# Performance work log

Measured on AMD Instinct MI355X. Metric: run time of the kernel, lower is better.

## Reference

```python
import jax, jax.numpy as jnp
import numpy as np

NUM_HEADS = 8
H_NUM, W_NUM = 1, 2   # idx=0 stripe windows
SCALE = float((256 // NUM_HEADS) ** -0.5)  # qk_scale


def _partition(x, h_sp, w_sp):
    # x: (T,B,C,H,W) -> (T, B*nWin, heads, N, C//heads) with N = h_sp*w_sp
    T, B, C, H, W = x.shape
    x = x.reshape(T, B, C, H // h_sp, h_sp, W // w_sp, w_sp)
    x = x.transpose(0, 1, 3, 5, 4, 6, 2)  # T,B,nH,nW,h_sp,w_sp,C
    x = x.reshape(T, -1, h_sp * w_sp, NUM_HEADS, C // NUM_HEADS)
    return x.transpose(0, 1, 3, 2, 4)


def setup_inputs() -> dict:
    key = jax.random.key(0)
    k1, k2, k3 = jax.random.split(key, 3)
    shape = (4, 2, 256, 56, 56)
    return {
        "q": jax.random.normal(k1, shape, jnp.float32),
        "k": jax.random.normal(k2, shape, jnp.float32),
        "v": jax.random.normal(k3, shape, jnp.float32),
        "v_lamda": 1,
    }


def reference(q, k, v, v_lamda):
    T, B, C, H0, W0 = q.shape
    h_pad = (-H0) % H_NUM
    w_pad = (-W0) % W_NUM
    pad = ((0, 0), (0, 0), (0, 0), (0, h_pad), (0, w_pad))
    q = jnp.pad(q, pad)
    k = jnp.pad(k, pad)
    v = jnp.pad(v, pad)
    H, W = H0 + h_pad, W0 + w_pad
    h_sp, w_sp = H // H_NUM, W // W_NUM

    qw = _partition(q, h_sp, w_sp)  # (T, BnW, h, N, d)
    kw = _partition(k, h_sp, w_sp)
    vw = _partition(v, h_sp, w_sp)  # head dim = C*v_lamda//heads

    attn = jnp.einsum('twhnd,twhmd->twhnm', qw, kw)          # (QK^T), no softmax
    out = jnp.einsum('twhnm,twhmd->twhnd', attn, vw) * (SCALE * 2)

    # merge windows back: (T,BnW,h,N,d) -> (T,B,Cv,H,W)
    Cv = C * v_lamda
    out = out.transpose(0, 1, 3, 2, 4).reshape(T, -1, h_sp * w_sp, Cv)
    out = out.reshape(T, B, H_NUM, W_NUM, h_sp, w_sp, Cv)
    out = out.transpose(0, 1, 2, 4, 3, 5, 6).reshape(T, B, H, W, Cv)
    out = out.transpose(0, 1, 4, 2, 3)
    return out[:, :, :, :H0, :W0]
```

## Files before the change

### kernel.cpp

```cpp
#include <hip/hip_runtime.h>


#define HW 3136
#define WDIM 56
#define SPLIT 14
#define PSPLIT 112
#define SCALE2 0.35355339059327373f

typedef const __attribute__((address_space(1))) void gas_void;
typedef __attribute__((address_space(3))) void las_void;
typedef float v2f __attribute__((ext_vector_type(2)));

__global__ __launch_bounds__(256, 4) void kv_kernel(const float* __restrict__ K,
                                                    const float* __restrict__ V,
                                                    float* __restrict__ Mpart) {
    __shared__ float lds[2 * 32 * PSPLIT];

    const int blk = blockIdx.x;
    const int p   = blk / SPLIT;
    const int s   = blk - p * SPLIT;
    const int head = p & 7;
    const int win  = (p >> 3) & 1;
    const int b    = (p >> 4) & 1;
    const int t    = p >> 5;

    const size_t base = (size_t)((t * 2 + b) * 256 + head * 32) * HW;
    const float* __restrict__ Kb = K + base;
    const float* __restrict__ Vb = V + base;

    const int tid = threadIdx.x;
    const int l   = tid & 63;
    const int w   = tid >> 6;

    #pragma unroll
    for (int i = 0; i < 7; ++i) {
        const int q    = (w * 7 + i) * 64 + l;
        const int isv  = q >= 896 ? 1 : 0;
        const int r    = q - isv * 896;
        const int pq   = r >> 5;
        const int slot = r & 31;
        const int ch   = ((slot & 7) << 2) + (slot >> 3);
        const int n    = s * PSPLIT + pq * 4;
        const int y    = n / 28;
        const int x    = n - y * 28;
        const float* src = (isv ? Vb : Kb)
                         + (size_t)ch * HW + y * WDIM + win * 28 + x;
        float* dst = &lds[(w * 7 + i) * 256];
        __builtin_amdgcn_global_load_lds((gas_void*)src, (las_void*)dst, 16, 0, 0);
    }
    __syncthreads();

    const int gg = l >> 3;
    const int e  = l & 7;

    v2f acc2[4][4] = {};
    #pragma unroll
    for (int j = 0; j < 7; ++j) {
        const int rowb = (7 * w + j) * 128;
        float4 ka[4], va[4];
        #pragma unroll
        for (int i = 0; i < 4; ++i) {
            ka[i] = *(const float4*)&lds[rowb + (gg + 8 * i) * 4];
            va[i] = *(const float4*)&lds[3584 + rowb + (e + 8 * i) * 4];
        }
        #pragma unroll
        for (int i = 0; i < 4; ++i) {
            const v2f ka_lo = {ka[i].x, ka[i].y};
            const v2f ka_hi = {ka[i].z, ka[i].w};
            #pragma unroll
            for (int jj = 0; jj < 4; ++jj) {
                const v2f va_lo = {va[jj].x, va[jj].y};
                const v2f va_hi = {va[jj].z, va[jj].w};
                acc2[i][jj] += ka_lo * va_lo;
                acc2[i][jj] += ka_hi * va_hi;
            }
        }
    }
    __syncthreads();

    const int dd0 = gg * 4;
    const int de0 = e * 4;
    #pragma unroll
    for (int i = 0; i < 4; ++i)
        #pragma unroll
        for (int jj = 0; jj < 4; ++jj)
            lds[w * 1024 + (dd0 + i) * 32 + (de0 + jj)] = acc2[i][jj].x + acc2[i][jj].y;
    __syncthreads();

    const float4 r0 = *(const float4*)&lds[tid * 4];
    const float4 r1 = *(const float4*)&lds[1024 + tid * 4];
    const float4 r2 = *(const float4*)&lds[2048 + tid * 4];
    const float4 r3 = *(const float4*)&lds[3072 + tid * 4];
    float4 o;
    o.x = r0.x + r1.x + r2.x + r3.x;
    o.y = r0.y + r1.y + r2.y + r3.y;
    o.z = r0.z + r1.z + r2.z + r3.z;
    o.w = r0.w + r1.w + r2.w + r3.w;
    *(float4*)&Mpart[(size_t)blk * 1024 + tid * 4] = o;
}

__global__ __launch_bounds__(256, 4) void qm_kernel(const float* __restrict__ Q,
                                                    const float* __restrict__ Mpart,
                                                    float* __restrict__ Out) {
    __shared__ float M[1024];
    const int blk = blockIdx.x;
    const int p   = blk / 7;
    const int c   = blk - p * 7;
    const int tid = threadIdx.x;

    const int head = p & 7;
    const int win  = (p >> 3) & 1;
    const int b    = (p >> 4) & 1;
    const int t    = p >> 5;

    const float* __restrict__ Qb = nullptr;
    float*       __restrict__ Ob = nullptr;
    float qv[32];
    if (tid < 224) {
        const int n = c * 224 + tid;
        const int y = n / 28;
        const int x = n - y * 28;
        const size_t base = (size_t)((t * 2 + b) * 256 + head * 32) * HW
                          + y * WDIM + win * 28 + x;
        Qb = Q + base;
        Ob = Out + base;
        #pragma unroll
        for (int dd = 0; dd < 32; ++dd)
            qv[dd] = Qb[(size_t)dd * HW];
    }

    const float* mp = Mpart + (size_t)p * SPLIT * 1024 + tid * 4;
    v2f s0 = {0.f, 0.f}, s1 = {0.f, 0.f};
    #pragma unroll
    for (int s = 0; s < SPLIT; ++s) {
        const float4 v = *(const float4*)&mp[s * 1024];
        const v2f vlo = {v.x, v.y};
        const v2f vhi = {v.z, v.w};
        s0 += vlo; s1 += vhi;
    }
    float4 sum;
    sum.x = s0.x * SCALE2; sum.y = s0.y * SCALE2;
    sum.z = s1.x * SCALE2; sum.w = s1.y * SCALE2;
    *(float4*)&M[tid * 4] = sum;
    __syncthreads();

    if (tid < 224) {
        v2f acc2[16] = {};
        #pragma unroll 8
        for (int dd = 0; dd < 32; ++dd) {
            const v2f qq = {qv[dd], qv[dd]};
            #pragma unroll
            for (int g4 = 0; g4 < 8; ++g4) {
                const float4 m = *(const float4*)&M[dd * 32 + g4 * 4];
                const v2f mlo = {m.x, m.y};
                const v2f mhi = {m.z, m.w};
                acc2[g4 * 2 + 0] += qq * mlo;
                acc2[g4 * 2 + 1] += qq * mhi;
            }
        }
        #pragma unroll
        for (int g4 = 0; g4 < 8; ++g4) {
            Ob[(size_t)(g4 * 4 + 0) * HW] = acc2[g4 * 2 + 0].x;
            Ob[(size_t)(g4 * 4 + 1) * HW] = acc2[g4 * 2 + 0].y;
            Ob[(size_t)(g4 * 4 + 2) * HW] = acc2[g4 * 2 + 1].x;
            Ob[(size_t)(g4 * 4 + 3) * HW] = acc2[g4 * 2 + 1].y;
        }
    }
}

extern "C" void kernel_launch(void* const* d_in, const int* in_sizes, int n_in,
                              void* d_out, int out_size, void* d_ws, size_t ws_size,
                              hipStream_t stream) {
    const float* q = (const float*)d_in[0];
    const float* k = (const float*)d_in[1];
    const float* v = (const float*)d_in[2];
    float* out   = (float*)d_out;
    float* Mpart = (float*)d_ws;

    kv_kernel<<<128 * SPLIT, 256, 0, stream>>>(k, v, Mpart);
    qm_kernel<<<128 * 7, 256, 0, stream>>>(q, Mpart, out);
}
```

Measured before the change: 127.8 us.

## Double KV split count, and process two pixels per thread in Q·M kernel

The K·V reduction kernel now splits each window-head into 28 chunks of 56 pixels instead of 14 chunks of 112, doubling its block count and halving its LDS footprint. The load and compute loops are reshaped to match. The second kernel now has each thread handle two adjacent pixels with 8-byte vector loads and stores, and uses 4 blocks per window-head instead of 7. The aim is more parallelism in the first kernel and wider memory accesses in the second, at the cost of twice as many partial sums to reduce and more registers per thread.

```diff
diff --git a/kernel.cpp b/kernel.cpp
--- a/kernel.cpp
+++ b/kernel.cpp
@@ -3,18 +3,18 @@
 
 #define HW 3136
 #define WDIM 56
-#define SPLIT 14
-#define PSPLIT 112
+#define SPLIT 28
+#define PSPLIT 56
 #define SCALE2 0.35355339059327373f
 
 typedef const __attribute__((address_space(1))) void gas_void;
 typedef __attribute__((address_space(3))) void las_void;
 typedef float v2f __attribute__((ext_vector_type(2)));
 
-__global__ __launch_bounds__(256, 4) void kv_kernel(const float* __restrict__ K,
-                                                    const float* __restrict__ V,
-                                                    float* __restrict__ Mpart) {
-    __shared__ float lds[2 * 32 * PSPLIT];
+__global__ __launch_bounds__(256) void kv_kernel(const float* __restrict__ K,
+                                                 const float* __restrict__ V,
+                                                 float* __restrict__ Mpart) {
+    __shared__ float lds[4096];
 
     const int blk = blockIdx.x;
     const int p   = blk / SPLIT;
@@ -33,20 +33,22 @@
     const int w   = tid >> 6;
 
     #pragma unroll
-    for (int i = 0; i < 7; ++i) {
-        const int q    = (w * 7 + i) * 64 + l;
-        const int isv  = q >= 896 ? 1 : 0;
-        const int r    = q - isv * 896;
-        const int pq   = r >> 5;
-        const int slot = r & 31;
-        const int ch   = ((slot & 7) << 2) + (slot >> 3);
-        const int n    = s * PSPLIT + pq * 4;
-        const int y    = n / 28;
-        const int x    = n - y * 28;
-        const float* src = (isv ? Vb : Kb)
-                         + (size_t)ch * HW + y * WDIM + win * 28 + x;
-        float* dst = &lds[(w * 7 + i) * 256];
-        __builtin_amdgcn_global_load_lds((gas_void*)src, (las_void*)dst, 16, 0, 0);
+    for (int i = 0; i < 4; ++i) {
+        if (i < 3 || w < 2) {
+            const int q    = i * 256 + tid;
+            const int isv  = q >= 448 ? 1 : 0;
+            const int r    = q - isv * 448;
+            const int pq   = r >> 5;
+            const int slot = r & 31;
+            const int ch   = ((slot & 7) << 2) + (slot >> 3);
+            const int n    = s * PSPLIT + pq * 4;
+            const int y    = n / 28;
+            const int x    = n - y * 28;
+            const float* src = (isv ? Vb : Kb)
+                             + (size_t)ch * HW + y * WDIM + win * 28 + x;
+            float* dst = &lds[i * 1024 + w * 256];
+            __builtin_amdgcn_global_load_lds((gas_void*)src, (las_void*)dst, 16, 0, 0);
+        }
     }
     __syncthreads();
 
@@ -55,24 +57,27 @@
 
     v2f acc2[4][4] = {};
     #pragma unroll
-    for (int j = 0; j < 7; ++j) {
-        const int rowb = (7 * w + j) * 128;
-        float4 ka[4], va[4];
-        #pragma unroll
-        for (int i = 0; i < 4; ++i) {
-            ka[i] = *(const float4*)&lds[rowb + (gg + 8 * i) * 4];
-            va[i] = *(const float4*)&lds[3584 + rowb + (e + 8 * i) * 4];
-        }
-        #pragma unroll
-        for (int i = 0; i < 4; ++i) {
-            const v2f ka_lo = {ka[i].x, ka[i].y};
-            const v2f ka_hi = {ka[i].z, ka[i].w};
+    for (int j = 0; j < 4; ++j) {
+        const int pq = w + 4 * j;
+        if (pq < 14) {
+            const int rowb = pq * 128;
+            float4 ka[4], va[4];
             #pragma unroll
-            for (int jj = 0; jj < 4; ++jj) {
-                const v2f va_lo = {va[jj].x, va[jj].y};
-                const v2f va_hi = {va[jj].z, va[jj].w};
-                acc2[i][jj] += ka_lo * va_lo;
-                acc2[i][jj] += ka_hi * va_hi;
+            for (int i = 0; i < 4; ++i) {
+                ka[i] = *(const float4*)&lds[rowb + (gg + 8 * i) * 4];
+                va[i] = *(const float4*)&lds[1792 + rowb + (e + 8 * i) * 4];
+            }
+            #pragma unroll
+            for (int i = 0; i < 4; ++i) {
+                const v2f ka_lo = {ka[i].x, ka[i].y};
+                const v2f ka_hi = {ka[i].z, ka[i].w};
+                #pragma unroll
+                for (int jj = 0; jj < 4; ++jj) {
+                    const v2f va_lo = {va[jj].x, va[jj].y};
+                    const v2f va_hi = {va[jj].z, va[jj].w};
+                    acc2[i][jj] += ka_lo * va_lo;
+                    acc2[i][jj] += ka_hi * va_hi;
+                }
             }
         }
     }
@@ -99,39 +104,18 @@
     *(float4*)&Mpart[(size_t)blk * 1024 + tid * 4] = o;
 }
 
-__global__ __launch_bounds__(256, 4) void qm_kernel(const float* __restrict__ Q,
-                                                    const float* __restrict__ Mpart,
-                                                    float* __restrict__ Out) {
+__global__ __launch_bounds__(256) void qm_kernel(const float* __restrict__ Q,
+                                                 const float* __restrict__ Mpart,
+                                                 float* __restrict__ Out) {
     __shared__ float M[1024];
     const int blk = blockIdx.x;
-    const int p   = blk / 7;
-    const int c   = blk - p * 7;
+    const int p   = blk >> 2;
+    const int c   = blk & 3;
     const int tid = threadIdx.x;
-
-    const int head = p & 7;
-    const int win  = (p >> 3) & 1;
-    const int b    = (p >> 4) & 1;
-    const int t    = p >> 5;
-
-    const float* __restrict__ Qb = nullptr;
-    float*       __restrict__ Ob = nullptr;
-    float qv[32];
-    if (tid < 224) {
-        const int n = c * 224 + tid;
-        const int y = n / 28;
-        const int x = n - y * 28;
-        const size_t base = (size_t)((t * 2 + b) * 256 + head * 32) * HW
-                          + y * WDIM + win * 28 + x;
-        Qb = Q + base;
-        Ob = Out + base;
-        #pragma unroll
-        for (int dd = 0; dd < 32; ++dd)
-            qv[dd] = Qb[(size_t)dd * HW];
-    }
 
     const float* mp = Mpart + (size_t)p * SPLIT * 1024 + tid * 4;
     v2f s0 = {0.f, 0.f}, s1 = {0.f, 0.f};
-    #pragma unroll
+    #pragma unroll 7
     for (int s = 0; s < SPLIT; ++s) {
         const float4 v = *(const float4*)&mp[s * 1024];
         const v2f vlo = {v.x, v.y};
@@ -144,27 +128,36 @@
     *(float4*)&M[tid * 4] = sum;
     __syncthreads();
 
-    if (tid < 224) {
-        v2f acc2[16] = {};
+    const int head = p & 7;
+    const int win  = (p >> 3) & 1;
+    const int b    = (p >> 4) & 1;
+    const int t    = p >> 5;
+
+    if (tid < 196) {
+        const int pr = c * 196 + tid;
+        const int y  = pr / 14;
+        const int x  = (pr - y * 14) * 2;
+        const size_t base = (size_t)((t * 2 + b) * 256 + head * 32) * HW
+                          + y * WDIM + win * 28 + x;
+        const float* __restrict__ Qb = Q + base;
+        float* __restrict__ Ob = Out + base;
+
+        v2f acc[32] = {};
         #pragma unroll 8
         for (int dd = 0; dd < 32; ++dd) {
-            const v2f qq = {qv[dd], qv[dd]};
+            const v2f qq = *(const v2f*)&Qb[(size_t)dd * HW];
             #pragma unroll
             for (int g4 = 0; g4 < 8; ++g4) {
                 const float4 m = *(const float4*)&M[dd * 32 + g4 * 4];
-                const v2f mlo = {m.x, m.y};
-                const v2f mhi = {m.z, m.w};
-                acc2[g4 * 2 + 0] += qq * mlo;
-                acc2[g4 * 2 + 1] += qq * mhi;
+                acc[g4 * 4 + 0] += qq * m.x;
+                acc[g4 * 4 + 1] += qq * m.y;
+                acc[g4 * 4 + 2] += qq * m.z;
+                acc[g4 * 4 + 3] += qq * m.w;
             }
         }
         #pragma unroll
-        for (int g4 = 0; g4 < 8; ++g4) {
-            Ob[(size_t)(g4 * 4 + 0) * HW] = acc2[g4 * 2 + 0].x;
-            Ob[(size_t)(g4 * 4 + 1) * HW] = acc2[g4 * 2 + 0].y;
-            Ob[(size_t)(g4 * 4 + 2) * HW] = acc2[g4 * 2 + 1].x;
-            Ob[(size_t)(g4 * 4 + 3) * HW] = acc2[g4 * 2 + 1].y;
-        }
+        for (int de = 0; de < 32; ++de)
+            *(v2f*)&Ob[(size_t)de * HW] = acc[de];
     }
 }
 
@@ -178,5 +171,5 @@
     float* Mpart = (float*)d_ws;
 
     kv_kernel<<<128 * SPLIT, 256, 0, stream>>>(k, v, Mpart);
-    qm_kernel<<<128 * 7, 256, 0, stream>>>(q, Mpart, out);
+    qm_kernel<<<128 * 4, 256, 0, stream>>>(q, Mpart, out);
 }
```

Result: slower. 133.7 us (+4.6%).
